# Kernel optimization log

Measured on AMD Instinct MI355X. Metric: run time of the kernel, lower is better.

Reference implementation:

```python
import jax, jax.numpy as jnp
import numpy as np

B, N, C, K = 4, 4096, 128, 16
LN_EPS = 1e-5


def knn(x, k):
    # x: [B,N,3] -> idx of k nearest (incl. self): [B,N,k]
    xx = jnp.sum(x * x, axis=2, keepdims=True)            # [B,N,1]
    inner = -2.0 * jnp.matmul(x, jnp.swapaxes(x, 1, 2))   # [B,N,N]
    pairwise = -xx - inner - jnp.swapaxes(xx, 1, 2)       # = -||xi-xj||^2
    _, idx = jax.lax.top_k(pairwise, k)                   # largest = nearest
    return idx


def index_points(points, idx):
    # points: [B,N,C], idx: [B,N,K] -> [B,N,K,C]
    return jax.vmap(lambda p, i: p[i])(points, idx)


def layer_norm(x, g, b):
    m = jnp.mean(x, axis=-1, keepdims=True)
    v = jnp.mean((x - m) ** 2, axis=-1, keepdims=True)
    return (x - m) * jax.lax.rsqrt(v + LN_EPS) * g + b


def setup_inputs() -> dict:
    key = jax.random.key(0)
    ks = jax.random.split(key, 16)
    h, q = C // 2, C // 4
    w = lambda k, s, sc: jax.random.normal(k, s, jnp.float32) * sc
    return dict(
        xyz=jax.random.normal(ks[0], (B, N, 3), jnp.float32),
        features=jax.random.normal(ks[1], (B, N, C), jnp.float32),
        geo_w1=w(ks[2], (10, h), 0.3), geo_b1=jnp.zeros((h,), jnp.float32),
        geo_g1=jnp.ones((h,), jnp.float32), geo_be1=jnp.zeros((h,), jnp.float32),
        geo_w2=w(ks[3], (h, h), 0.12), geo_b2=jnp.zeros((h,), jnp.float32),
        diff_w1=w(ks[4], (C, h), 0.09), diff_b1=jnp.zeros((h,), jnp.float32),
        diff_g1=jnp.ones((h,), jnp.float32), diff_be1=jnp.zeros((h,), jnp.float32),
        diff_w2=w(ks[5], (h, h), 0.12), diff_b2=jnp.zeros((h,), jnp.float32),
        ep_w1=w(ks[6], (C, q), 0.09), ep_b1=jnp.zeros((q,), jnp.float32),
        ep_w2=w(ks[7], (q, 1), 0.17), ep_b2=jnp.zeros((1,), jnp.float32),
        ref_w1=w(ks[8], (2 * C, C), 0.06), ref_b1=jnp.zeros((C,), jnp.float32),
        ref_g1=jnp.ones((C,), jnp.float32), ref_be1=jnp.zeros((C,), jnp.float32),
    )


def reference(xyz, features,
              geo_w1, geo_b1, geo_g1, geo_be1, geo_w2, geo_b2,
              diff_w1, diff_b1, diff_g1, diff_be1, diff_w2, diff_b2,
              ep_w1, ep_b1, ep_w2, ep_b2,
              ref_w1, ref_b1, ref_g1, ref_be1):
    # --- geometric features ---
    idx = knn(xyz, K)                                    # [B,N,K]
    neighbors = index_points(xyz, idx)                   # [B,N,K,3]
    rel_pos = neighbors - xyz[:, :, None, :]             # [B,N,K,3]
    cov = jnp.einsum('bnkc,bnkd->bncd', rel_pos, rel_pos) / K  # [B,N,3,3]
    _, eigvecs = jnp.linalg.eigh(cov)                    # ascending eigenvalues
    normal = eigvecs[..., :, 0]                          # smallest-eig direction
    curvature_dir = eigvecs[..., :, 2]                   # largest-eig direction
    mean_rel = jnp.mean(rel_pos, axis=2)                 # [B,N,3]
    mean_dist = jnp.mean(jnp.linalg.norm(rel_pos, axis=-1), axis=-1, keepdims=True)
    geo_feat = jnp.concatenate([normal, curvature_dir, mean_rel, mean_dist], axis=-1)  # [B,N,10]

    geo_h = layer_norm(geo_feat @ geo_w1 + geo_b1, geo_g1, geo_be1)
    geo_encoded = jax.nn.relu(geo_h) @ geo_w2 + geo_b2   # [B,N,C/2]

    # --- feature differences (knn recomputed as in the original) ---
    idx2 = knn(xyz, K)
    neighbor_feats = index_points(features, idx2)        # [B,N,K,C]
    feat_diff = jnp.mean(jnp.abs(features[:, :, None, :] - neighbor_feats), axis=2)  # [B,N,C]
    diff_h = layer_norm(feat_diff @ diff_w1 + diff_b1, diff_g1, diff_be1)
    diff_encoded = jax.nn.relu(diff_h) @ diff_w2 + diff_b2

    # --- edge probability + refinement ---
    edge_feat = jnp.concatenate([geo_encoded, diff_encoded], axis=-1)  # [B,N,C]
    ep_h = jax.nn.relu(edge_feat @ ep_w1 + ep_b1)
    edge_prob = jax.nn.sigmoid(ep_h @ ep_w2 + ep_b2)     # [B,N,1]

    enhanced = jnp.concatenate([features, edge_feat * edge_prob], axis=-1)  # [B,N,2C]
    refined = jax.nn.relu(layer_norm(enhanced @ ref_w1 + ref_b1, ref_g1, ref_be1))
    refined = refined + features                          # dropout in eval mode = identity
    return refined, edge_prob
```

## Files before the change

kernel.cpp:

```cpp
#include <hip/hip_runtime.h>
#include <hip/hip_bf16.h>

#define N_ 4096
#define C_ 128
#define K_ 16
#define NPT 16384

__device__ __forceinline__ float wave_sum64(float v) {
#pragma unroll
  for (int off = 32; off >= 1; off >>= 1) v += __shfl_xor(v, off, 64);
  return v;
}


__device__ __forceinline__ float sign_f(float a, float b) {
  return copysignf(fabsf(a), b);
}

__device__ float lapy2_f(float x, float y) {
#pragma clang fp contract(off)
  float xa = fabsf(x), ya = fabsf(y);
  float w = fmaxf(xa, ya), z = fminf(xa, ya);
  if (z == 0.0f) return w;
  float t = z / w;
  return w * sqrtf(1.0f + t * t);
}

__device__ void lartg_f(float f, float g, float& c, float& s, float& r) {
#pragma clang fp contract(off)
  if (g == 0.0f) {
    c = 1.0f; s = 0.0f; r = f;
  } else if (f == 0.0f) {
    c = 0.0f; s = copysignf(1.0f, g); r = fabsf(g);
  } else {
    float d = sqrtf(f * f + g * g);
    c = fabsf(f) / d;
    r = sign_f(d, f);
    s = g / r;
  }
}

__device__ void laev2_f(float a, float b, float cc, float& rt1, float& rt2,
                        float& cs1, float& sn1) {
#pragma clang fp contract(off)
  float sm = a + cc;
  float df = a - cc;
  float adf = fabsf(df);
  float tb = b + b;
  float ab = fabsf(tb);
  float acmx, acmn;
  if (fabsf(a) > fabsf(cc)) { acmx = a; acmn = cc; } else { acmx = cc; acmn = a; }
  float rt;
  if (adf > ab) {
    float t = ab / adf; rt = adf * sqrtf(1.0f + t * t);
  } else if (adf < ab) {
    float t = adf / ab; rt = ab * sqrtf(1.0f + t * t);
  } else {
    rt = ab * sqrtf(2.0f);
  }
  int sgn1;
  if (sm < 0.0f) {
    rt1 = 0.5f * (sm - rt); sgn1 = -1;
    rt2 = (acmx / rt1) * acmn - (b / rt1) * b;
  } else if (sm > 0.0f) {
    rt1 = 0.5f * (sm + rt); sgn1 = 1;
    rt2 = (acmx / rt1) * acmn - (b / rt1) * b;
  } else {
    rt1 = 0.5f * rt; rt2 = -0.5f * rt; sgn1 = 1;
  }
  float cs; int sgn2;
  if (df >= 0.0f) { cs = df + rt; sgn2 = 1; } else { cs = df - rt; sgn2 = -1; }
  float acs = fabsf(cs);
  if (acs > ab) {
    float ct = -tb / cs;
    sn1 = 1.0f / sqrtf(1.0f + ct * ct);
    cs1 = ct * sn1;
  } else {
    if (ab == 0.0f) { cs1 = 1.0f; sn1 = 0.0f; }
    else {
      float tn = -cs / tb;
      cs1 = 1.0f / sqrtf(1.0f + tn * tn);
      sn1 = tn * cs1;
    }
  }
  if (sgn1 == sgn2) { float tn = cs1; cs1 = -sn1; sn1 = tn; }
}

__device__ void steqr3_f(float d[3], float e[2], float Z[3][3]) {
#pragma clang fp contract(off)
  const int n = 3;
  const float eps = 5.9604644775390625e-08f;
  const float eps2 = eps * eps;
  const float safmin = 1.17549435e-38f;
  const int nmaxit = n * 30;
  int jtot = 0;
  int l1 = 1;

  for (int og = 0; og < 16; ++og) {
    if (l1 > n) break;
    if (l1 > 1) e[l1 - 2] = 0.0f;
    int m, l, lend;
    if (l1 <= n - 1) {
      bool found = false;
      for (m = l1; m <= n - 1; ++m) {
        float tst = fabsf(e[m - 1]);
        if (tst == 0.0f) { found = true; break; }
        if (tst <= (sqrtf(fabsf(d[m - 1])) * sqrtf(fabsf(d[m]))) * eps) {
          e[m - 1] = 0.0f; found = true; break;
        }
      }
      if (!found) m = n;
    } else {
      m = n;
    }
    l = l1; lend = m; l1 = m + 1;
    if (lend == l) continue;
    if (fabsf(d[lend - 1]) < fabsf(d[l - 1])) { int t = l; l = lend; lend = t; }

    if (lend > l) {
      for (int it = 0; it < 128; ++it) {
        int mm;
        if (l != lend) {
          bool f2 = false;
          for (mm = l; mm <= lend - 1; ++mm) {
            float tst = e[mm - 1] * e[mm - 1];
            if (tst <= (eps2 * fabsf(d[mm - 1])) * fabsf(d[mm]) + safmin) { f2 = true; break; }
          }
          if (!f2) mm = lend;
        } else mm = lend;
        if (mm < lend) e[mm - 1] = 0.0f;
        float p = d[l - 1];
        if (mm == l) {
          d[l - 1] = p; ++l;
          if (l <= lend) continue;
          break;
        }
        if (mm == l + 1) {
          float rt1, rt2, cc, ss;
          laev2_f(d[l - 1], e[l - 1], d[l], rt1, rt2, cc, ss);
          for (int r = 0; r < n; ++r) {
            float temp = Z[r][l];
            Z[r][l] = cc * temp - ss * Z[r][l - 1];
            Z[r][l - 1] = ss * temp + cc * Z[r][l - 1];
          }
          d[l - 1] = rt1; d[l] = rt2; e[l - 1] = 0.0f;
          l += 2;
          if (l <= lend) continue;
          break;
        }
        if (jtot == nmaxit) break;
        ++jtot;
        float g = (d[l] - p) / (2.0f * e[l - 1]);
        float r = lapy2_f(g, 1.0f);
        g = d[mm - 1] - p + e[l - 1] / (g + sign_f(r, g));
        float s = 1.0f, c = 1.0f;
        p = 0.0f;
        float csv[2], snv[2];
        for (int i = mm - 1; i >= l; --i) {
          float f = s * e[i - 1];
          float bb = c * e[i - 1];
          lartg_f(g, f, c, s, r);
          if (i != mm - 1) e[i] = r;
          g = d[i] - p;
          r = (d[i - 1] - g) * s + 2.0f * c * bb;
          p = s * r;
          d[i] = g + p;
          g = c * r - bb;
          csv[i - l] = c;
          snv[i - l] = -s;
        }
        int mml = mm - l;
        for (int j = mml; j >= 1; --j) {
          float cc = csv[j - 1], ss = snv[j - 1];
          for (int r2 = 0; r2 < n; ++r2) {
            float temp = Z[r2][l + j - 1];
            Z[r2][l + j - 1] = cc * temp - ss * Z[r2][l + j - 2];
            Z[r2][l + j - 2] = ss * temp + cc * Z[r2][l + j - 2];
          }
        }
        d[l - 1] -= p;
        e[l - 1] = g;
      }
    } else {
      for (int it = 0; it < 128; ++it) {
        int mm;
        if (l != lend) {
          bool f2 = false;
          for (mm = l; mm >= lend + 1; --mm) {
            float tst = e[mm - 2] * e[mm - 2];
            if (tst <= (eps2 * fabsf(d[mm - 1])) * fabsf(d[mm - 2]) + safmin) { f2 = true; break; }
          }
          if (!f2) mm = lend;
        } else mm = lend;
        if (mm > lend) e[mm - 2] = 0.0f;
        float p = d[l - 1];
        if (mm == l) {
          d[l - 1] = p; --l;
          if (l >= lend) continue;
          break;
        }
        if (mm == l - 1) {
          float rt1, rt2, cc, ss;
          laev2_f(d[l - 2], e[l - 2], d[l - 1], rt1, rt2, cc, ss);
          for (int r = 0; r < n; ++r) {
            float temp = Z[r][l - 1];
            Z[r][l - 1] = cc * temp - ss * Z[r][l - 2];
            Z[r][l - 2] = ss * temp + cc * Z[r][l - 2];
          }
          d[l - 2] = rt1; d[l - 1] = rt2; e[l - 2] = 0.0f;
          l -= 2;
          if (l >= lend) continue;
          break;
        }
        if (jtot == nmaxit) break;
        ++jtot;
        float g = (d[l - 2] - p) / (2.0f * e[l - 2]);
        float r = lapy2_f(g, 1.0f);
        g = d[mm - 1] - p + e[l - 2] / (g + sign_f(r, g));
        float s = 1.0f, c = 1.0f;
        p = 0.0f;
        float csv[2], snv[2];
        for (int i = mm; i <= l - 1; ++i) {
          float f = s * e[i - 1];
          float bb = c * e[i - 1];
          lartg_f(g, f, c, s, r);
          if (i != mm) e[i - 2] = r;
          g = d[i - 1] - p;
          r = (d[i] - g) * s + 2.0f * c * bb;
          p = s * r;
          d[i - 1] = g + p;
          g = c * r - bb;
          csv[i - mm] = c;
          snv[i - mm] = s;
        }
        int lm = l - mm;
        for (int j = 1; j <= lm; ++j) {
          float cc = csv[j - 1], ss = snv[j - 1];
          for (int r2 = 0; r2 < n; ++r2) {
            float temp = Z[r2][mm + j - 1];
            Z[r2][mm + j - 1] = cc * temp - ss * Z[r2][mm + j - 2];
            Z[r2][mm + j - 2] = ss * temp + cc * Z[r2][mm + j - 2];
          }
        }
        d[l - 1] -= p;
        e[l - 2] = g;
      }
    }
  }
  for (int ii = 2; ii <= n; ++ii) {
    int i = ii - 1, k = i;
    float p = d[i - 1];
    for (int j = ii; j <= n; ++j) {
      if (d[j - 1] < p) { k = j; p = d[j - 1]; }
    }
    if (k != i) {
      d[k - 1] = d[i - 1]; d[i - 1] = p;
      for (int r = 0; r < n; ++r) {
        float t = Z[r][i - 1]; Z[r][i - 1] = Z[r][k - 1]; Z[r][k - 1] = t;
      }
    }
  }
}

__device__ void eig3_f(float A00, float A10, float A20,
                       float A11, float A21, float A22, float Z[3][3]) {
#pragma clang fp contract(off)
  float d[3], e[2];
  float tau = 0.0f, v2 = 0.0f;
  d[0] = A00;
  float xnorm = fabsf(A20);
  if (xnorm == 0.0f) {
    tau = 0.0f; v2 = 0.0f;
    e[0] = A10; d[1] = A11; e[1] = A21; d[2] = A22;
  } else {
    float beta = -sign_f(lapy2_f(A10, xnorm), A10);
    tau = (beta - A10) / beta;
    float inv = 1.0f / (A10 - beta);
    v2 = A20 * inv;
    e[0] = beta;
    float x0 = tau * A11;
    float x1 = tau * A21;
    float tmp2 = A21 * v2;
    x0 = x0 + tau * tmp2;
    x1 = x1 + (tau * v2) * A22;
    float dotv = x0 + x1 * v2;
    float aw = (-0.5f * tau) * dotv;
    float w0 = x0 + aw;
    float w1 = x1 + aw * v2;
    d[1] = (A11 - w0) - w0;
    float pq = v2 * w0;
    e[1] = (A21 - pq) - w1;
    float pr = v2 * w1;
    d[2] = (A22 - pr) - pr;
  }
  Z[0][0] = 1.0f; Z[0][1] = 0.0f; Z[0][2] = 0.0f;
  Z[1][0] = 0.0f; Z[1][1] = 1.0f; Z[1][2] = 0.0f;
  Z[2][0] = 0.0f; Z[2][1] = 0.0f; Z[2][2] = 1.0f;
  steqr3_f(d, e, Z);
  if (tau != 0.0f) {
    for (int j = 0; j < 3; ++j) {
      float sum = Z[1][j] + v2 * Z[2][j];
      float tw = tau * sum;
      Z[1][j] = Z[1][j] - tw;
      Z[2][j] = Z[2][j] - v2 * tw;
    }
  }
}

__device__ __forceinline__ unsigned long long knn_key(float qx, float qy, float qz,
                                                      float nqxx, float x, float y,
                                                      float z, int j) {
  const float dot = __fmaf_rn(qz, z, __fmaf_rn(qy, y, __fmul_rn(qx, x)));
  const float xxj =
      __fadd_rn(__fadd_rn(__fmul_rn(x, x), __fmul_rn(y, y)), __fmul_rn(z, z));
  const float inner = __fmul_rn(-2.0f, dot);
  const float pval = __fsub_rn(__fsub_rn(nqxx, inner), xxj);
  const unsigned bits = __float_as_uint(pval);
  const unsigned ordv = bits ^ (unsigned)(((int)bits >> 31) | 0x80000000);
  return ((unsigned long long)ordv << 32) | (unsigned)(4095 - j);
}

__global__ __launch_bounds__(256, 6) void knn_kernel(const float* __restrict__ xyz,
                                                     int* __restrict__ nidx_ws) {
  __shared__ struct { float xs[1024]; float ys[1024]; float zs[1024]; } soa;

  const int wave = threadIdx.x >> 6;
  const int lane = threadIdx.x & 63;
  const int tid = threadIdx.x;
  const int P0 = blockIdx.x * 8;
  const int b = P0 >> 12;
  const int r0 = P0 & 4095;
  const int pbase = r0 + wave * 2;
  const float* xb = xyz + (size_t)b * (N_ * 3);

  float qx[2], qy[2], qz[2], nqxx[2];
#pragma unroll
  for (int q = 0; q < 2; ++q) {
    const int i = pbase + q;
    qx[q] = xb[3 * i]; qy[q] = xb[3 * i + 1]; qz[q] = xb[3 * i + 2];
    nqxx[q] = -__fadd_rn(__fadd_rn(__fmul_rn(qx[q], qx[q]), __fmul_rn(qy[q], qy[q])),
                         __fmul_rn(qz[q], qz[q]));
  }

  unsigned long long pk[2][4];
#pragma unroll
  for (int q = 0; q < 2; ++q)
#pragma unroll
    for (int s = 0; s < 4; ++s) pk[q][s] = 0ull;

  for (int tile = 0; tile < 4; ++tile) {
    {
      const float4* gsrc = (const float4*)(xb + tile * 3072);
      float4 a0 = gsrc[tid * 3];
      float4 a1 = gsrc[tid * 3 + 1];
      float4 a2 = gsrc[tid * 3 + 2];
      const int qq = tid * 4;
      soa.xs[qq] = a0.x; soa.xs[qq + 1] = a0.w; soa.xs[qq + 2] = a1.z; soa.xs[qq + 3] = a2.y;
      soa.ys[qq] = a0.y; soa.ys[qq + 1] = a1.x; soa.ys[qq + 2] = a1.w; soa.ys[qq + 3] = a2.z;
      soa.zs[qq] = a0.z; soa.zs[qq + 1] = a1.y; soa.zs[qq + 2] = a2.x; soa.zs[qq + 3] = a2.w;
    }
    __syncthreads();

#pragma unroll 2
    for (int tloc = 0; tloc < 16; ++tloc) {
      const int idx = tloc * 64 + lane;
      const int j = tile * 1024 + idx;
      const float x = soa.xs[idx];
      const float y = soa.ys[idx];
      const float z = soa.zs[idx];
      const float xxj =
          __fadd_rn(__fadd_rn(__fmul_rn(x, x), __fmul_rn(y, y)), __fmul_rn(z, z));
      const unsigned jenc = (unsigned)(4095 - j);
#pragma unroll
      for (int q = 0; q < 2; ++q) {
        const float dot =
            __fmaf_rn(qz[q], z, __fmaf_rn(qy[q], y, __fmul_rn(qx[q], x)));
        const float inner = __fmul_rn(-2.0f, dot);
        const float pval = __fsub_rn(__fsub_rn(nqxx[q], inner), xxj);
        const unsigned bits = __float_as_uint(pval);
        const unsigned ordv = bits ^ (unsigned)(((int)bits >> 31) | 0x80000000);
        const unsigned long long key = ((unsigned long long)ordv << 32) | jenc;
        const bool c0 = key > pk[q][0], c1 = key > pk[q][1],
                   c2 = key > pk[q][2], c3 = key > pk[q][3];
        pk[q][3] = c3 ? (c2 ? pk[q][2] : key) : pk[q][3];
        pk[q][2] = c2 ? (c1 ? pk[q][1] : key) : pk[q][2];
        pk[q][1] = c1 ? (c0 ? pk[q][0] : key) : pk[q][1];
        pk[q][0] = c0 ? key : pk[q][0];
      }
    }
    __syncthreads();
  }

  int stash[2];
  int h[2] = {0, 0};
#pragma unroll
  for (int k = 0; k < K_; ++k) {
    unsigned long long v[2];
#pragma unroll
    for (int q = 0; q < 2; ++q) v[q] = pk[q][0];
#pragma unroll
    for (int off = 32; off >= 1; off >>= 1) {
#pragma unroll
      for (int q = 0; q < 2; ++q) {
        unsigned long long ov = __shfl_xor(v[q], off, 64);
        if (ov > v[q]) v[q] = ov;
      }
    }
#pragma unroll
    for (int q = 0; q < 2; ++q) {
      const int jidx = (4095 - (int)(unsigned)(v[q] & 0xFFFFFFFFull)) & (N_ - 1);
      if (lane == k) stash[q] = jidx;
      if (pk[q][0] == v[q]) {
        pk[q][0] = pk[q][1]; pk[q][1] = pk[q][2]; pk[q][2] = pk[q][3];
        pk[q][3] = 0ull;
        ++h[q];
      }
    }
  }
#pragma unroll
  for (int q = 0; q < 2; ++q) {
    if (__ballot(h[q] >= 4) != 0ull) {
      unsigned long long qq[K_];
#pragma unroll
      for (int k = 0; k < K_; ++k) qq[k] = 0ull;
      for (int t = 0; t < 64; ++t) {
        const int j = t * 64 + lane;
        const unsigned long long key = knn_key(qx[q], qy[q], qz[q], nqxx[q],
                                               xb[3 * j], xb[3 * j + 1],
                                               xb[3 * j + 2], j);
        bool c[K_];
#pragma unroll
        for (int s = 0; s < K_; ++s) c[s] = key > qq[s];
#pragma unroll
        for (int s = K_ - 1; s >= 1; --s)
          qq[s] = c[s] ? (c[s - 1] ? qq[s - 1] : key) : qq[s];
        qq[0] = c[0] ? key : qq[0];
      }
#pragma unroll
      for (int k = 0; k < K_; ++k) {
        unsigned long long v = qq[0];
#pragma unroll
        for (int off = 32; off >= 1; off >>= 1) {
          unsigned long long ov = __shfl_xor(v, off, 64);
          if (ov > v) v = ov;
        }
        const int jidx = (4095 - (int)(unsigned)(v & 0xFFFFFFFFull)) & (N_ - 1);
        if (lane == k) stash[q] = jidx;
        if (qq[0] == v) {
#pragma unroll
          for (int s = 0; s < K_ - 1; ++s) qq[s] = qq[s + 1];
          qq[K_ - 1] = 0ull;
        }
      }
    }
  }

  if (lane < K_) {
    const int pg = P0 + wave * 2;
#pragma unroll
    for (int q = 0; q < 2; ++q)
      nidx_ws[(size_t)(pg + q) * K_ + lane] = stash[q];
  }
}

__global__ __launch_bounds__(64) void eig_kernel(const float* __restrict__ xyz,
                                                 const int* __restrict__ nidx_ws,
                                                 float* __restrict__ gf_ws) {
  const int p = blockIdx.x * 64 + threadIdx.x;
  const int b = p >> 12;
  const int i = p & 4095;
  const float* xb = xyz + (size_t)b * (N_ * 3);
  const float qx = xb[3 * i];
  const float qy = xb[3 * i + 1];
  const float qz = xb[3 * i + 2];

  int nidx[K_];
#pragma unroll
  for (int k = 0; k < K_; ++k) nidx[k] = nidx_ws[(size_t)p * K_ + k];

  float c00 = 0, c01 = 0, c02 = 0, c11 = 0, c12 = 0, c22 = 0;
  float mrx = 0, mry = 0, mrz = 0, md = 0;
#pragma unroll
  for (int k = 0; k < K_; ++k) {
    const int j = nidx[k];
    const float rx = __fsub_rn(xb[3 * j], qx);
    const float ry = __fsub_rn(xb[3 * j + 1], qy);
    const float rz = __fsub_rn(xb[3 * j + 2], qz);
    c00 = __fadd_rn(c00, __fmul_rn(rx, rx));
    c01 = __fadd_rn(c01, __fmul_rn(rx, ry));
    c02 = __fadd_rn(c02, __fmul_rn(rx, rz));
    c11 = __fadd_rn(c11, __fmul_rn(ry, ry));
    c12 = __fadd_rn(c12, __fmul_rn(ry, rz));
    c22 = __fadd_rn(c22, __fmul_rn(rz, rz));
    mrx = __fadd_rn(mrx, rx);
    mry = __fadd_rn(mry, ry);
    mrz = __fadd_rn(mrz, rz);
    const float nn = __fadd_rn(__fadd_rn(__fmul_rn(rx, rx), __fmul_rn(ry, ry)),
                               __fmul_rn(rz, rz));
    md = __fadd_rn(md, sqrtf(nn));
  }
  const float s16 = 0.0625f;
  float Z[3][3];
  eig3_f(__fmul_rn(c00, s16), __fmul_rn(c01, s16), __fmul_rn(c02, s16),
         __fmul_rn(c11, s16), __fmul_rn(c12, s16), __fmul_rn(c22, s16), Z);
  float* g = gf_ws + (size_t)p * 12;
  g[0] = Z[0][0]; g[1] = Z[1][0]; g[2] = Z[2][0];
  g[3] = Z[0][2]; g[4] = Z[1][2]; g[5] = Z[2][2];
  g[6] = __fmul_rn(mrx, s16); g[7] = __fmul_rn(mry, s16);
  g[8] = __fmul_rn(mrz, s16);
  g[9] = __fmul_rn(md, s16);
}

__global__ __launch_bounds__(256) void mlp_kernel(
    const float* __restrict__ feats, const int* __restrict__ nidx_ws,
    const float* __restrict__ gf_ws,
    const float* __restrict__ geo_w1, const float* __restrict__ geo_b1,
    const float* __restrict__ geo_g1, const float* __restrict__ geo_be1,
    const float* __restrict__ geo_w2, const float* __restrict__ geo_b2,
    const float* __restrict__ diff_w1, const float* __restrict__ diff_b1,
    const float* __restrict__ diff_g1, const float* __restrict__ diff_be1,
    const float* __restrict__ diff_w2, const float* __restrict__ diff_b2,
    const float* __restrict__ ep_w1, const float* __restrict__ ep_b1,
    const float* __restrict__ ep_w2, const float* __restrict__ ep_b2,
    const float* __restrict__ ref_w1, const float* __restrict__ ref_b1,
    const float* __restrict__ ref_g1, const float* __restrict__ ref_be1,
    float* __restrict__ out, float* __restrict__ out_prob) {

  __shared__ float w[8192];
  __shared__ float fsh[16 * 128];
  __shared__ float sdif[16 * 128];
  __shared__ float ysh[16 * 64];
  __shared__ float edsh[16 * 128];
  __shared__ float insh[16 * 12];
  __shared__ int nsh[16 * 16];

  const int tid = threadIdx.x;
  const int lane = tid & 63;
  const int g = tid >> 6;
  const int P0 = blockIdx.x * 16;
  const int b = P0 >> 12;
  const int r0 = P0 & 4095;
  const float* fb = feats + (size_t)b * N_ * C_;

  if (tid < 192) insh[tid] = gf_ws[(size_t)P0 * 12 + tid];
  nsh[tid] = nidx_ws[(size_t)P0 * K_ + tid];
#pragma unroll
  for (int m = 0; m < 8; ++m)
    fsh[m * 256 + tid] = fb[(size_t)r0 * C_ + m * 256 + tid];
  if (tid < 160) ((float4*)w)[tid] = ((const float4*)geo_w1)[tid];
#pragma unroll
  for (int m = 0; m < 4; ++m)
    ((float4*)(w + 640))[m * 256 + tid] = ((const float4*)geo_w2)[m * 256 + tid];
  __syncthreads();

  {
    float acc[4] = {0, 0, 0, 0};
#pragma unroll
    for (int c = 0; c < 10; ++c) {
      const float wv = w[c * 64 + lane];
#pragma unroll
      for (int ptl = 0; ptl < 4; ++ptl)
        acc[ptl] += insh[(g * 4 + ptl) * 12 + c] * wv;
    }
#pragma unroll
    for (int ptl = 0; ptl < 4; ++ptl) {
      const int pt = g * 4 + ptl;
      float a = acc[ptl] + geo_b1[lane];
      float m = wave_sum64(a) * (1.0f / 64.0f);
      float xm = a - m;
      float var = wave_sum64(xm * xm) * (1.0f / 64.0f);
      float yv = xm * (1.0f / sqrtf(var + 1e-5f)) * geo_g1[lane] + geo_be1[lane];
      ysh[pt * 64 + lane] = fmaxf(yv, 0.0f);
    }
  }
  __syncthreads();

  float ge[4] = {0, 0, 0, 0}, de[4], prob[4];
#pragma unroll 4
  for (int c = 0; c < 64; ++c) {
    const float wv = w[640 + c * 64 + lane];
#pragma unroll
    for (int ptl = 0; ptl < 4; ++ptl)
      ge[ptl] += ysh[(g * 4 + ptl) * 64 + c] * wv;
  }
#pragma unroll
  for (int ptl = 0; ptl < 4; ++ptl) ge[ptl] += geo_b2[lane];

  {
    const int h2 = tid >> 7, c = tid & 127;
    for (int ptp = 0; ptp < 8; ++ptp) {
      const int pt = h2 * 8 + ptp;
      const float fv = fsh[pt * 128 + c];
      float s = 0.0f;
#pragma unroll
      for (int k = 0; k < K_; ++k) {
        const int j = nsh[pt * 16 + k];
        s += fabsf(fv - fb[(size_t)j * C_ + c]);
      }
      sdif[pt * 128 + c] = s * (1.0f / 16.0f);
    }
  }
  __syncthreads();
#pragma unroll
  for (int m = 0; m < 8; ++m)
    ((float4*)w)[m * 256 + tid] = ((const float4*)diff_w1)[m * 256 + tid];
  __syncthreads();

  {
    float acc[4] = {0, 0, 0, 0};
#pragma unroll 4
    for (int c = 0; c < 128; ++c) {
      const float wv = w[c * 64 + lane];
#pragma unroll
      for (int ptl = 0; ptl < 4; ++ptl)
        acc[ptl] += sdif[(g * 4 + ptl) * 128 + c] * wv;
    }
#pragma unroll
    for (int ptl = 0; ptl < 4; ++ptl) {
      const int pt = g * 4 + ptl;
      float a = acc[ptl] + diff_b1[lane];
      float m = wave_sum64(a) * (1.0f / 64.0f);
      float xm = a - m;
      float var = wave_sum64(xm * xm) * (1.0f / 64.0f);
      float yv = xm * (1.0f / sqrtf(var + 1e-5f)) * diff_g1[lane] + diff_be1[lane];
      ysh[pt * 64 + lane] = fmaxf(yv, 0.0f);
    }
  }
  __syncthreads();
#pragma unroll
  for (int m = 0; m < 4; ++m)
    ((float4*)w)[m * 256 + tid] = ((const float4*)diff_w2)[m * 256 + tid];
#pragma unroll
  for (int m = 0; m < 4; ++m)
    ((float4*)w)[1024 + m * 256 + tid] = ((const float4*)ep_w1)[m * 256 + tid];
  __syncthreads();

  {
    float acc[4] = {0, 0, 0, 0};
#pragma unroll 4
    for (int c = 0; c < 64; ++c) {
      const float wv = w[c * 64 + lane];
#pragma unroll
      for (int ptl = 0; ptl < 4; ++ptl)
        acc[ptl] += ysh[(g * 4 + ptl) * 64 + c] * wv;
    }
#pragma unroll
    for (int ptl = 0; ptl < 4; ++ptl) {
      const int pt = g * 4 + ptl;
      de[ptl] = acc[ptl] + diff_b2[lane];
      edsh[pt * 128 + lane] = ge[ptl];
      edsh[pt * 128 + 64 + lane] = de[ptl];
    }
  }
  __syncthreads();

  const int u = lane & 31;
  {
    float ea[4] = {0, 0, 0, 0};
#pragma unroll 4
    for (int c = 0; c < 128; ++c) {
      const float wv = w[4096 + c * 32 + u];
#pragma unroll
      for (int ptl = 0; ptl < 4; ++ptl)
        ea[ptl] += edsh[(g * 4 + ptl) * 128 + c] * wv;
    }
#pragma unroll
    for (int ptl = 0; ptl < 4; ++ptl) {
      float a = ea[ptl] + ep_b1[u];
      float hh = (lane < 32) ? fmaxf(a, 0.0f) * ep_w2[u] : 0.0f;
      float tsum = wave_sum64(hh) + ep_b2[0];
      prob[ptl] = 1.0f / (1.0f + expf(-tsum));
    }
  }
  __syncthreads();
#pragma unroll
  for (int ptl = 0; ptl < 4; ++ptl) {
    const int pt = g * 4 + ptl;
    edsh[pt * 128 + lane] = ge[ptl] * prob[ptl];
    edsh[pt * 128 + 64 + lane] = de[ptl] * prob[ptl];
  }

  float a0[4] = {0, 0, 0, 0}, a1[4] = {0, 0, 0, 0};
  for (int ch = 0; ch < 4; ++ch) {
    __syncthreads();
    {
      const float4* gsrc = (const float4*)(ref_w1 + ch * 8192);
#pragma unroll
      for (int m = 0; m < 8; ++m) ((float4*)w)[m * 256 + tid] = gsrc[m * 256 + tid];
    }
    __syncthreads();
#pragma unroll 4
    for (int cl = 0; cl < 64; ++cl) {
      const float w0 = w[cl * 128 + lane];
      const float w1v = w[cl * 128 + 64 + lane];
#pragma unroll
      for (int ptl = 0; ptl < 4; ++ptl) {
        const int pt = g * 4 + ptl;
        const float e = (ch < 2) ? fsh[pt * 128 + ch * 64 + cl]
                                 : edsh[pt * 128 + (ch - 2) * 64 + cl];
        a0[ptl] += e * w0;
        a1[ptl] += e * w1v;
      }
    }
  }

#pragma unroll
  for (int ptl = 0; ptl < 4; ++ptl) {
    const int pt = g * 4 + ptl;
    float A0 = a0[ptl] + ref_b1[lane];
    float A1 = a1[ptl] + ref_b1[64 + lane];
    float mm2 = wave_sum64(A0 + A1) * (1.0f / 128.0f);
    float d0 = A0 - mm2, d1 = A1 - mm2;
    float var2 = wave_sum64(d0 * d0 + d1 * d1) * (1.0f / 128.0f);
    float rs = 1.0f / sqrtf(var2 + 1e-5f);
    float y0 = d0 * rs * ref_g1[lane] + ref_be1[lane];
    float y1 = d1 * rs * ref_g1[64 + lane] + ref_be1[64 + lane];
    y0 = fmaxf(y0, 0.0f) + fsh[pt * 128 + lane];
    y1 = fmaxf(y1, 0.0f) + fsh[pt * 128 + 64 + lane];
    out[(size_t)(P0 + pt) * 128 + lane] = y0;
    out[(size_t)(P0 + pt) * 128 + 64 + lane] = y1;
    if (lane == 0) out_prob[P0 + pt] = prob[ptl];
  }
}

__global__ __launch_bounds__(256) void fused_kernel(
    const float* __restrict__ xyz, const float* __restrict__ feats,
    const float* __restrict__ geo_w1, const float* __restrict__ geo_b1,
    const float* __restrict__ geo_g1, const float* __restrict__ geo_be1,
    const float* __restrict__ geo_w2, const float* __restrict__ geo_b2,
    const float* __restrict__ diff_w1, const float* __restrict__ diff_b1,
    const float* __restrict__ diff_g1, const float* __restrict__ diff_be1,
    const float* __restrict__ diff_w2, const float* __restrict__ diff_b2,
    const float* __restrict__ ep_w1, const float* __restrict__ ep_b1,
    const float* __restrict__ ep_w2, const float* __restrict__ ep_b2,
    const float* __restrict__ ref_w1, const float* __restrict__ ref_b1,
    const float* __restrict__ ref_g1, const float* __restrict__ ref_be1,
    float* __restrict__ out, float* __restrict__ out_prob) {

  __shared__ float4 tile4[1024];

  const int wave = threadIdx.x >> 6;
  const int lane = threadIdx.x & 63;
  const int tid = threadIdx.x;
  const int p = blockIdx.x * 4 + wave;
  const int b = p >> 12;
  const int i = p & 4095;
  const float* xb = xyz + (size_t)b * (N_ * 3);

  const float qx = xb[3 * i];
  const float qy = xb[3 * i + 1];
  const float qz = xb[3 * i + 2];
  const float qxx =
      __fadd_rn(__fadd_rn(__fmul_rn(qx, qx), __fmul_rn(qy, qy)), __fmul_rn(qz, qz));
  const float nqxx = -qxx;

  unsigned long long pk[4] = {0ull, 0ull, 0ull, 0ull};
  for (int tile = 0; tile < 4; ++tile) {
    {
      const float4* gsrc = (const float4*)(xb + tile * 3072);
      float4 r0v = gsrc[tid * 3];
      float4 r1 = gsrc[tid * 3 + 1];
      float4 r2 = gsrc[tid * 3 + 2];
      const int base = tid * 4;
      tile4[base]     = make_float4(r0v.x, r0v.y, r0v.z, 0.0f);
      tile4[base + 1] = make_float4(r0v.w, r1.x, r1.y, 0.0f);
      tile4[base + 2] = make_float4(r1.z, r1.w, r2.x, 0.0f);
      tile4[base + 3] = make_float4(r2.y, r2.z, r2.w, 0.0f);
    }
    __syncthreads();
#pragma unroll 4
    for (int tloc = 0; tloc < 16; ++tloc) {
      const int j = tile * 1024 + tloc * 64 + lane;
      const float4 pt = tile4[tloc * 64 + lane];
      const unsigned long long key = knn_key(qx, qy, qz, nqxx, pt.x, pt.y, pt.z, j);
      const bool c0 = key > pk[0], c1 = key > pk[1], c2 = key > pk[2], c3 = key > pk[3];
      pk[3] = c3 ? (c2 ? pk[2] : key) : pk[3];
      pk[2] = c2 ? (c1 ? pk[1] : key) : pk[2];
      pk[1] = c1 ? (c0 ? pk[0] : key) : pk[1];
      pk[0] = c0 ? key : pk[0];
    }
    __syncthreads();
  }

  int nidx[K_];
  int h = 0;
#pragma unroll
  for (int k = 0; k < K_; ++k) {
    unsigned long long v = pk[0];
#pragma unroll
    for (int off = 32; off >= 1; off >>= 1) {
      unsigned long long ov = __shfl_xor(v, off, 64);
      if (ov > v) v = ov;
    }
    nidx[k] = (4095 - (int)(unsigned)(v & 0xFFFFFFFFull)) & (N_ - 1);
    if (pk[0] == v) {
      pk[0] = pk[1]; pk[1] = pk[2]; pk[2] = pk[3]; pk[3] = 0ull;
      ++h;
    }
  }
  if (__ballot(h >= 4) != 0ull) {
    unsigned long long q[K_];
#pragma unroll
    for (int k = 0; k < K_; ++k) q[k] = 0ull;
    for (int t = 0; t < 64; ++t) {
      const int j = t * 64 + lane;
      const unsigned long long key =
          knn_key(qx, qy, qz, nqxx, xb[3 * j], xb[3 * j + 1], xb[3 * j + 2], j);
      bool c[K_];
#pragma unroll
      for (int s = 0; s < K_; ++s) c[s] = key > q[s];
#pragma unroll
      for (int s = K_ - 1; s >= 1; --s)
        q[s] = c[s] ? (c[s - 1] ? q[s - 1] : key) : q[s];
      q[0] = c[0] ? key : q[0];
    }
#pragma unroll
    for (int k = 0; k < K_; ++k) {
      unsigned long long v = q[0];
#pragma unroll
      for (int off = 32; off >= 1; off >>= 1) {
        unsigned long long ov = __shfl_xor(v, off, 64);
        if (ov > v) v = ov;
      }
      nidx[k] = (4095 - (int)(unsigned)(v & 0xFFFFFFFFull)) & (N_ - 1);
      if (q[0] == v) {
#pragma unroll
        for (int s = 0; s < K_ - 1; ++s) q[s] = q[s + 1];
        q[K_ - 1] = 0ull;
      }
    }
  }

  float c00 = 0, c01 = 0, c02 = 0, c11 = 0, c12 = 0, c22 = 0;
  float mrx = 0, mry = 0, mrz = 0, md = 0;
#pragma unroll
  for (int k = 0; k < K_; ++k) {
    const int j = nidx[k];
    const float rx = __fsub_rn(xb[3 * j], qx);
    const float ry = __fsub_rn(xb[3 * j + 1], qy);
    const float rz = __fsub_rn(xb[3 * j + 2], qz);
    c00 = __fadd_rn(c00, __fmul_rn(rx, rx));
    c01 = __fadd_rn(c01, __fmul_rn(rx, ry));
    c02 = __fadd_rn(c02, __fmul_rn(rx, rz));
    c11 = __fadd_rn(c11, __fmul_rn(ry, ry));
    c12 = __fadd_rn(c12, __fmul_rn(ry, rz));
    c22 = __fadd_rn(c22, __fmul_rn(rz, rz));
    mrx = __fadd_rn(mrx, rx);
    mry = __fadd_rn(mry, ry);
    mrz = __fadd_rn(mrz, rz);
    const float nn = __fadd_rn(__fadd_rn(__fmul_rn(rx, rx), __fmul_rn(ry, ry)),
                               __fmul_rn(rz, rz));
    md = __fadd_rn(md, sqrtf(nn));
  }
  const float s16 = 0.0625f;
  float Z[3][3];
  eig3_f(__fmul_rn(c00, s16), __fmul_rn(c01, s16), __fmul_rn(c02, s16),
         __fmul_rn(c11, s16), __fmul_rn(c12, s16), __fmul_rn(c22, s16), Z);
  float gf[10];
  gf[0] = Z[0][0]; gf[1] = Z[1][0]; gf[2] = Z[2][0];
  gf[3] = Z[0][2]; gf[4] = Z[1][2]; gf[5] = Z[2][2];
  gf[6] = __fmul_rn(mrx, s16); gf[7] = __fmul_rn(mry, s16);
  gf[8] = __fmul_rn(mrz, s16);
  gf[9] = __fmul_rn(md, s16);

  float acc = 0.0f;
#pragma unroll
  for (int ii = 0; ii < 10; ++ii) acc += gf[ii] * geo_w1[ii * 64 + lane];
  acc += geo_b1[lane];
  float yr;
  {
    float m = wave_sum64(acc) * (1.0f / 64.0f);
    float xm = acc - m;
    float var = wave_sum64(xm * xm) * (1.0f / 64.0f);
    float yv = xm * (1.0f / sqrtf(var + 1e-5f)) * geo_g1[lane] + geo_be1[lane];
    yr = fmaxf(yv, 0.0f);
  }
  float ge = 0.0f;
#pragma unroll 8
  for (int jj = 0; jj < 64; ++jj) ge += __shfl(yr, jj, 64) * geo_w2[jj * 64 + lane];
  ge += geo_b2[lane];

  const float* fb = feats + (size_t)b * N_ * C_;
  const float* fi = fb + (size_t)i * C_;
  const float f0 = fi[lane];
  const float f1 = fi[64 + lane];
  float s0 = 0.0f, s1 = 0.0f;
#pragma unroll
  for (int k = 0; k < K_; ++k) {
    const float* fj = fb + (size_t)nidx[k] * C_;
    s0 += fabsf(f0 - fj[lane]);
    s1 += fabsf(f1 - fj[64 + lane]);
  }
  s0 *= (1.0f / 16.0f);
  s1 *= (1.0f / 16.0f);
  float acc2 = 0.0f;
#pragma unroll 8
  for (int c = 0; c < 64; ++c) acc2 += __shfl(s0, c, 64) * diff_w1[c * 64 + lane];
#pragma unroll 8
  for (int c = 64; c < 128; ++c) acc2 += __shfl(s1, c - 64, 64) * diff_w1[c * 64 + lane];
  acc2 += diff_b1[lane];
  float yr2;
  {
    float m = wave_sum64(acc2) * (1.0f / 64.0f);
    float xm = acc2 - m;
    float var = wave_sum64(xm * xm) * (1.0f / 64.0f);
    float yv = xm * (1.0f / sqrtf(var + 1e-5f)) * diff_g1[lane] + diff_be1[lane];
    yr2 = fmaxf(yv, 0.0f);
  }
  float de = 0.0f;
#pragma unroll 8
  for (int jj = 0; jj < 64; ++jj) de += __shfl(yr2, jj, 64) * diff_w2[jj * 64 + lane];
  de += diff_b2[lane];

  {
    const int u = lane & 31;
    float a = 0.0f;
#pragma unroll 8
    for (int c = 0; c < 64; ++c) a += __shfl(ge, c, 64) * ep_w1[c * 32 + u];
#pragma unroll 8
    for (int c = 64; c < 128; ++c) a += __shfl(de, c - 64, 64) * ep_w1[c * 32 + u];
    a += ep_b1[u];
    float hh = (lane < 32) ? fmaxf(a, 0.0f) * ep_w2[u] : 0.0f;
    float tsum = wave_sum64(hh) + ep_b2[0];
    float prob = 1.0f / (1.0f + expf(-tsum));

    const float gep = ge * prob;
    const float dep = de * prob;
    float a0 = 0.0f, a1 = 0.0f;
#pragma unroll 4
    for (int c = 0; c < 64; ++c) {
      float ec = __shfl(f0, c, 64);
      a0 += ec * ref_w1[c * 128 + lane];
      a1 += ec * ref_w1[c * 128 + 64 + lane];
    }
#pragma unroll 4
    for (int c = 64; c < 128; ++c) {
      float ec = __shfl(f1, c - 64, 64);
      a0 += ec * ref_w1[c * 128 + lane];
      a1 += ec * ref_w1[c * 128 + 64 + lane];
    }
#pragma unroll 4
    for (int c = 128; c < 192; ++c) {
      float ec = __shfl(gep, c - 128, 64);
      a0 += ec * ref_w1[c * 128 + lane];
      a1 += ec * ref_w1[c * 128 + 64 + lane];
    }
#pragma unroll 4
    for (int c = 192; c < 256; ++c) {
      float ec = __shfl(dep, c - 192, 64);
      a0 += ec * ref_w1[c * 128 + lane];
      a1 += ec * ref_w1[c * 128 + 64 + lane];
    }
    a0 += ref_b1[lane];
    a1 += ref_b1[64 + lane];
    float mm2 = wave_sum64(a0 + a1) * (1.0f / 128.0f);
    float d0 = a0 - mm2, d1 = a1 - mm2;
    float var2 = wave_sum64(d0 * d0 + d1 * d1) * (1.0f / 128.0f);
    float rs = 1.0f / sqrtf(var2 + 1e-5f);
    float y0 = d0 * rs * ref_g1[lane] + ref_be1[lane];
    float y1 = d1 * rs * ref_g1[64 + lane] + ref_be1[64 + lane];
    y0 = fmaxf(y0, 0.0f) + f0;
    y1 = fmaxf(y1, 0.0f) + f1;
    out[(size_t)p * 128 + lane] = y0;
    out[(size_t)p * 128 + 64 + lane] = y1;
    if (lane == 0) out_prob[p] = prob;
  }
}

extern "C" void kernel_launch(void* const* d_in, const int* in_sizes, int n_in,
                              void* d_out, int out_size, void* d_ws, size_t ws_size,
                              hipStream_t stream) {
  const float* xyz = (const float*)d_in[0];
  const float* features = (const float*)d_in[1];
  const float* geo_w1 = (const float*)d_in[2];
  const float* geo_b1 = (const float*)d_in[3];
  const float* geo_g1 = (const float*)d_in[4];
  const float* geo_be1 = (const float*)d_in[5];
  const float* geo_w2 = (const float*)d_in[6];
  const float* geo_b2 = (const float*)d_in[7];
  const float* diff_w1 = (const float*)d_in[8];
  const float* diff_b1 = (const float*)d_in[9];
  const float* diff_g1 = (const float*)d_in[10];
  const float* diff_be1 = (const float*)d_in[11];
  const float* diff_w2 = (const float*)d_in[12];
  const float* diff_b2 = (const float*)d_in[13];
  const float* ep_w1 = (const float*)d_in[14];
  const float* ep_b1 = (const float*)d_in[15];
  const float* ep_w2 = (const float*)d_in[16];
  const float* ep_b2 = (const float*)d_in[17];
  const float* ref_w1 = (const float*)d_in[18];
  const float* ref_b1 = (const float*)d_in[19];
  const float* ref_g1 = (const float*)d_in[20];
  const float* ref_be1 = (const float*)d_in[21];

  float* out = (float*)d_out;
  float* out_prob = out + (size_t)NPT * C_;

  if (ws_size >= (size_t)(2 * 1024 * 1024)) {
    int* nidx_ws = (int*)d_ws;
    float* gf_ws = (float*)((char*)d_ws + (1u << 20));
    knn_kernel<<<dim3(NPT / 8), dim3(256), 0, stream>>>(xyz, nidx_ws);
    eig_kernel<<<dim3(NPT / 64), dim3(64), 0, stream>>>(xyz, nidx_ws, gf_ws);
    mlp_kernel<<<dim3(NPT / 16), dim3(256), 0, stream>>>(
        features, nidx_ws, gf_ws, geo_w1, geo_b1, geo_g1, geo_be1, geo_w2,
        geo_b2, diff_w1, diff_b1, diff_g1, diff_be1, diff_w2, diff_b2, ep_w1,
        ep_b1, ep_w2, ep_b2, ref_w1, ref_b1, ref_g1, ref_be1, out, out_prob);
  } else {
    fused_kernel<<<dim3(NPT / 4), dim3(256), 0, stream>>>(
        xyz, features, geo_w1, geo_b1, geo_g1, geo_be1, geo_w2, geo_b2,
        diff_w1, diff_b1, diff_g1, diff_be1, diff_w2, diff_b2, ep_w1, ep_b1,
        ep_w2, ep_b2, ref_w1, ref_b1, ref_g1, ref_be1, out, out_prob);
  }
}
```

Before: 324.6 us.

## Defer KNN overflow fallback to a separate fixup kernel via flagged list

The rare full-scan fallback inside the KNN kernel, used when a lane's 4-entry candidate list overflows, is moved out of the main kernel. Flagged points are appended to a global list with an atomic counter, and a new fixup kernel recomputes them. The change also raises the occupancy hint from 6 to 8 and the inner loop unroll from 2 to 4, since the main kernel no longer carries the 16-entry register queue. It costs an extra memset and kernel launch, and it raises the workspace threshold to 3 MB, so the fused fallback path runs if the workspace is smaller.

```diff
diff --git a/kernel.cpp b/kernel.cpp
--- a/kernel.cpp
+++ b/kernel.cpp
@@ -320,8 +320,10 @@
   return ((unsigned long long)ordv << 32) | (unsigned)(4095 - j);
 }
 
-__global__ __launch_bounds__(256, 6) void knn_kernel(const float* __restrict__ xyz,
-                                                     int* __restrict__ nidx_ws) {
+__global__ __launch_bounds__(256, 8) void knn_kernel(const float* __restrict__ xyz,
+                                                     int* __restrict__ nidx_ws,
+                                                     int* __restrict__ flag_cnt,
+                                                     int* __restrict__ flag_list) {
   __shared__ struct { float xs[1024]; float ys[1024]; float zs[1024]; } soa;
 
   const int wave = threadIdx.x >> 6;
@@ -361,7 +363,7 @@
     }
     __syncthreads();
 
-#pragma unroll 2
+#pragma unroll 4
     for (int tloc = 0; tloc < 16; ++tloc) {
       const int idx = tloc * 64 + lane;
       const int j = tile * 1024 + idx;
@@ -420,37 +422,9 @@
 #pragma unroll
   for (int q = 0; q < 2; ++q) {
     if (__ballot(h[q] >= 4) != 0ull) {
-      unsigned long long qq[K_];
-#pragma unroll
-      for (int k = 0; k < K_; ++k) qq[k] = 0ull;
-      for (int t = 0; t < 64; ++t) {
-        const int j = t * 64 + lane;
-        const unsigned long long key = knn_key(qx[q], qy[q], qz[q], nqxx[q],
-                                               xb[3 * j], xb[3 * j + 1],
-                                               xb[3 * j + 2], j);
-        bool c[K_];
-#pragma unroll
-        for (int s = 0; s < K_; ++s) c[s] = key > qq[s];
-#pragma unroll
-        for (int s = K_ - 1; s >= 1; --s)
-          qq[s] = c[s] ? (c[s - 1] ? qq[s - 1] : key) : qq[s];
-        qq[0] = c[0] ? key : qq[0];
-      }
-#pragma unroll
-      for (int k = 0; k < K_; ++k) {
-        unsigned long long v = qq[0];
-#pragma unroll
-        for (int off = 32; off >= 1; off >>= 1) {
-          unsigned long long ov = __shfl_xor(v, off, 64);
-          if (ov > v) v = ov;
-        }
-        const int jidx = (4095 - (int)(unsigned)(v & 0xFFFFFFFFull)) & (N_ - 1);
-        if (lane == k) stash[q] = jidx;
-        if (qq[0] == v) {
-#pragma unroll
-          for (int s = 0; s < K_ - 1; ++s) qq[s] = qq[s + 1];
-          qq[K_ - 1] = 0ull;
-        }
+      if (lane == 0) {
+        const int slot = atomicAdd(flag_cnt, 1);
+        flag_list[slot & (NPT - 1)] = P0 + wave * 2 + q;
       }
     }
   }
@@ -460,6 +434,61 @@
 #pragma unroll
     for (int q = 0; q < 2; ++q)
       nidx_ws[(size_t)(pg + q) * K_ + lane] = stash[q];
+  }
+}
+
+__global__ __launch_bounds__(256) void knn_fixup_kernel(
+    const float* __restrict__ xyz, const int* __restrict__ flag_cnt,
+    const int* __restrict__ flag_list, int* __restrict__ nidx_ws) {
+  const int lane = threadIdx.x & 63;
+  const int wave_g = (blockIdx.x * 256 + threadIdx.x) >> 6;
+  const int total_waves = gridDim.x * 4;
+  const int n = min(*flag_cnt, NPT);
+
+  for (int idx = wave_g; idx < n; idx += total_waves) {
+    const int p = flag_list[idx];
+    const int b = p >> 12;
+    const int i = p & 4095;
+    const float* xb = xyz + (size_t)b * (N_ * 3);
+    const float qx = xb[3 * i];
+    const float qy = xb[3 * i + 1];
+    const float qz = xb[3 * i + 2];
+    const float nqxx =
+        -__fadd_rn(__fadd_rn(__fmul_rn(qx, qx), __fmul_rn(qy, qy)), __fmul_rn(qz, qz));
+
+    unsigned long long qq[K_];
+#pragma unroll
+    for (int k = 0; k < K_; ++k) qq[k] = 0ull;
+    for (int t = 0; t < 64; ++t) {
+      const int j = t * 64 + lane;
+      const unsigned long long key =
+          knn_key(qx, qy, qz, nqxx, xb[3 * j], xb[3 * j + 1], xb[3 * j + 2], j);
+      bool c[K_];
+#pragma unroll
+      for (int s = 0; s < K_; ++s) c[s] = key > qq[s];
+#pragma unroll
+      for (int s = K_ - 1; s >= 1; --s)
+        qq[s] = c[s] ? (c[s - 1] ? qq[s - 1] : key) : qq[s];
+      qq[0] = c[0] ? key : qq[0];
+    }
+    int stash = 0;
+#pragma unroll
+    for (int k = 0; k < K_; ++k) {
+      unsigned long long v = qq[0];
+#pragma unroll
+      for (int off = 32; off >= 1; off >>= 1) {
+        unsigned long long ov = __shfl_xor(v, off, 64);
+        if (ov > v) v = ov;
+      }
+      const int jidx = (4095 - (int)(unsigned)(v & 0xFFFFFFFFull)) & (N_ - 1);
+      if (lane == k) stash = jidx;
+      if (qq[0] == v) {
+#pragma unroll
+        for (int s = 0; s < K_ - 1; ++s) qq[s] = qq[s + 1];
+        qq[K_ - 1] = 0ull;
+      }
+    }
+    if (lane < K_) nidx_ws[(size_t)p * K_ + lane] = stash;
   }
 }
 
@@ -996,10 +1025,16 @@
   float* out = (float*)d_out;
   float* out_prob = out + (size_t)NPT * C_;
 
-  if (ws_size >= (size_t)(2 * 1024 * 1024)) {
+  if (ws_size >= (size_t)(3 * 1024 * 1024)) {
     int* nidx_ws = (int*)d_ws;
     float* gf_ws = (float*)((char*)d_ws + (1u << 20));
-    knn_kernel<<<dim3(NPT / 8), dim3(256), 0, stream>>>(xyz, nidx_ws);
+    int* flag_cnt = (int*)((char*)d_ws + (2u << 20));
+    int* flag_list = (int*)((char*)d_ws + (2u << 20) + 256);
+    hipMemsetAsync(flag_cnt, 0, 4, stream);
+    knn_kernel<<<dim3(NPT / 8), dim3(256), 0, stream>>>(xyz, nidx_ws, flag_cnt,
+                                                        flag_list);
+    knn_fixup_kernel<<<dim3(64), dim3(256), 0, stream>>>(xyz, flag_cnt,
+                                                         flag_list, nidx_ws);
     eig_kernel<<<dim3(NPT / 64), dim3(64), 0, stream>>>(xyz, nidx_ws, gf_ws);
     mlp_kernel<<<dim3(NPT / 16), dim3(256), 0, stream>>>(
         features, nidx_ws, gf_ws, geo_w1, geo_b1, geo_g1, geo_be1, geo_w2,
```

Result: slower. 335.7 us (+3.4%).
